# Optimization experiments

Measured on AMD Instinct MI355X. Metric: run time of the kernel, lower is better.

## Reference

```python
import jax, jax.numpy as jnp
import numpy as np

B, T, N, C_IN = 2, 12, 50000, 1
H = 16          # hidden = out channels of STConv
KT = 3          # temporal kernel size
E = 800000      # edges (avg degree 16)
NUM_CLASSES = 2


def _temporal_conv(x, wP, bP, wQ, bQ, wR, bR):
    # Gated temporal conv (GLU): relu(P * sigmoid(Q) + R), 'valid' conv over time.
    # x: (B, Tt, N, C); w*: (KT, C, H)
    Tt = x.shape[1]
    def conv(w, b):
        out = b
        for k in range(KT):  # KT=3, tiny unrolled loop
            out = out + jnp.einsum('btnc,co->btno', x[:, k:Tt - KT + 1 + k], w[k])
        return out
    return jax.nn.relu(conv(wP, bP) * jax.nn.sigmoid(conv(wQ, bQ)) + conv(wR, bR))


def _cheb_conv(x, edge_index, edge_weight, w, b):
    # ChebConv K=2, sym normalization, lambda_max=2:
    #   out  = Tx_0 @ W0 + Tx_1 @ W1 + b
    src, dst = edge_index[0], edge_index[1]
    n = x.shape[2]
    deg = jax.ops.segment_sum(edge_weight, src, num_segments=n)
    dis = jnp.where(deg > 0, jax.lax.rsqrt(jnp.maximum(deg, 1e-12)), 0.0)
    norm = -dis[src] * edge_weight * dis[dst]                    # (E,)
    Bc, Tc, _, Hc = x.shape
    xf = jnp.transpose(x, (2, 0, 1, 3)).reshape(n, -1)           # (N, B*T*H)
    agg = jax.ops.segment_sum(norm[:, None] * xf[src], dst, num_segments=n)
    tx1 = jnp.transpose(agg.reshape(n, Bc, Tc, Hc), (1, 2, 0, 3))  # (B, T, N, H)
    return jnp.einsum('btnc,co->btno', x, w[0]) + jnp.einsum('btnc,co->btno', tx1, w[1]) + b


def _forward(x, edge_index, edge_weight,
             tc1_P_w, tc1_P_b, tc1_Q_w, tc1_Q_b, tc1_R_w, tc1_R_b,
             cheb_w, cheb_b,
             tc2_P_w, tc2_P_b, tc2_Q_w, tc2_Q_b, tc2_R_w, tc2_R_b,
             lin_w, lin_b):
    h = _temporal_conv(x, tc1_P_w, tc1_P_b, tc1_Q_w, tc1_Q_b, tc1_R_w, tc1_R_b)  # (B, T-2, N, H)
    h = jax.nn.relu(_cheb_conv(h, edge_index, edge_weight, cheb_w, cheb_b))
    h = _temporal_conv(h, tc2_P_w, tc2_P_b, tc2_Q_w, tc2_Q_b, tc2_R_w, tc2_R_b)  # (B, T-4, N, H)
    h = h.mean(axis=1)                                                            # (B, N, H)
    return h @ lin_w + lin_b                                                      # (B, N, classes)


def setup_inputs() -> dict:
    key = jax.random.key(0)
    ks = jax.random.split(key, 12)
    x = jax.random.normal(ks[0], (B, T, N, C_IN), jnp.float32)
    edge_index = jax.random.randint(ks[1], (2, E), 0, N, dtype=jnp.int32).astype(jnp.int64)
    edge_weight = jax.random.uniform(ks[2], (E,), jnp.float32)

    def conv_w(k, cin, cout):
        s = 1.0 / np.sqrt(cin * KT)
        return jax.random.uniform(k, (KT, cin, cout), jnp.float32, -s, s)

    inp = {'x': x, 'edge_index': edge_index, 'edge_weight': edge_weight}
    for i, name in enumerate(['tc1_P', 'tc1_Q', 'tc1_R']):
        inp[name + '_w'] = conv_w(ks[3 + i], C_IN, H)
        inp[name + '_b'] = jnp.zeros((H,), jnp.float32)
    for i, name in enumerate(['tc2_P', 'tc2_Q', 'tc2_R']):
        inp[name + '_w'] = conv_w(ks[6 + i], H, H)
        inp[name + '_b'] = jnp.zeros((H,), jnp.float32)
    sc = 1.0 / np.sqrt(H)
    inp['cheb_w'] = jax.random.uniform(ks[9], (2, H, H), jnp.float32, -sc, sc)
    inp['cheb_b'] = jnp.zeros((H,), jnp.float32)
    inp['lin_w'] = jax.random.uniform(ks[10], (H, NUM_CLASSES), jnp.float32, -sc, sc)
    inp['lin_b'] = jnp.zeros((NUM_CLASSES,), jnp.float32)
    return inp


def reference(x, edge_index, edge_weight,
              tc1_P_w, tc1_P_b, tc1_Q_w, tc1_Q_b, tc1_R_w, tc1_R_b,
              tc2_P_w, tc2_P_b, tc2_Q_w, tc2_Q_b, tc2_R_w, tc2_R_b,
              cheb_w, cheb_b, lin_w, lin_b):
    return _forward(x, edge_index, edge_weight,
                    tc1_P_w, tc1_P_b, tc1_Q_w, tc1_Q_b, tc1_R_w, tc1_R_b,
                    cheb_w, cheb_b,
                    tc2_P_w, tc2_P_b, tc2_Q_w, tc2_Q_b, tc2_R_w, tc2_R_b,
                    lin_w, lin_b)
```

## Files before the change

### kernel.cpp

```cpp
#include <hip/hip_runtime.h>

typedef unsigned short ushort_t;
typedef unsigned int uint_t;
typedef __attribute__((ext_vector_type(8))) short short8;
typedef __attribute__((ext_vector_type(4))) float float4v;

constexpr int Bb = 2, Tt = 12, Nn = 50000, Hh = 16, Ee = 800000;
constexpr int T1 = 10, T2 = 8;
constexpr int F = 320;
constexpr int NP = 50176;
constexpr int NXCD = 8;
constexpr int CAP8 = 16;

#define DEV __device__ __forceinline__

DEV float bf2f(ushort_t u) { return __uint_as_float(((uint_t)u) << 16); }
DEV ushort_t f2bf(float f) {
  uint_t u = __float_as_uint(f);
  u += 0x7fffu + ((u >> 16) & 1u);
  return (ushort_t)(u >> 16);
}
DEV float blo(uint_t u) { return __uint_as_float(u << 16); }
DEV float bhi(uint_t u) { return __uint_as_float(u & 0xffff0000u); }
DEV float sigm(float x) { return 1.0f / (1.0f + __expf(-x)); }

DEV int xcc_id() {
  int x;
  asm volatile("s_getreg_b32 %0, hwreg(HW_REG_XCC_ID)" : "=s"(x));
  return x & (NXCD - 1);
}

DEV float loadF(const void* p, int j, int isb) {
  return isb ? bf2f(((const ushort_t*)p)[j]) : ((const float*)p)[j];
}
DEV int loadI(const void* p, long long j, int is64) {
  return is64 ? (int)(((const long long*)p)[j]) : ((const int*)p)[j];
}

__global__ void k_wprep(const void* ew, const void* ei,
                        const void* t1Pw, const void* t1Pb,
                        const void* t1Qw, const void* t1Qb,
                        const void* t1Rw, const void* t1Rb,
                        const void* t2Pw, const void* t2Pb,
                        const void* t2Qw, const void* t2Qb,
                        const void* t2Rw, const void* t2Rb,
                        const void* chw, const void* chb,
                        const void* lw, const void* lb,
                        int* flags, float* W, ushort_t* Bf, uint_t* zero_base) {
  int gid = blockIdx.x * 256 + threadIdx.x;
  if (gid < 16 * NP) zero_base[gid] = 0u;
  if (blockIdx.x != 0) return;

  __shared__ int sflags[2];
  int tid = threadIdx.x;
  if (tid < 64) {
    int lane = tid;
    const ushort_t* u = (const ushort_t*)ew;
    int cnt = 0;
    for (int j = lane; j < 512; j += 64) cnt += (u[j] < 0x3F80u) ? 1 : 0;
#pragma unroll
    for (int d = 32; d; d >>= 1) cnt += __shfl_xor(cnt, d, 64);
    const int* e32 = (const int*)ei;
    int even_nz = 0, odd_nz = 0;
    for (int j = 2 * lane; j < 256; j += 128) {
      even_nz |= (e32[j] != 0);
      odd_nz |= (e32[j + 1] != 0);
    }
    unsigned long long be = __ballot(even_nz), bo = __ballot(odd_nz);
    if (lane == 0) {
      int f0 = (cnt >= 450) ? 1 : 0;
      int f1 = (bo == 0ull && be != 0ull) ? 1 : 0;
      sflags[0] = f0; sflags[1] = f1;
      flags[0] = f0; flags[1] = f1;
    }
  }
  __syncthreads();
  int isb = sflags[0];
#define CVT(src, off, n) for (int j = tid; j < (n); j += 256) W[(off) + j] = loadF(src, j, isb);
  CVT(t1Pw, 0, 48)   CVT(t1Pb, 48, 16)
  CVT(t1Qw, 64, 48)  CVT(t1Qb, 112, 16)
  CVT(t1Rw, 128, 48) CVT(t1Rb, 176, 16)
  CVT(t2Pw, 192, 768)  CVT(t2Pb, 960, 16)
  CVT(t2Qw, 976, 768)  CVT(t2Qb, 1744, 16)
  CVT(t2Rw, 1760, 768) CVT(t2Rb, 2528, 16)
  CVT(chw, 2544, 512)  CVT(chb, 3056, 16)
  CVT(lw, 3072, 32)    CVT(lb, 3104, 2)
#undef CVT
  for (int i = tid; i < 3072; i += 256) {
    int j = i & 7, lane = (i >> 3) & 63, s = (i >> 9) & 1, tau = i >> 10;
    int kap = s * 32 + ((lane >> 4) << 3) + j;
    int nsub = lane & 15;
    ushort_t v = 0;
    if (kap < 48) {
      int kk = kap >> 4, c = kap & 15;
      const void* src = (tau == 0) ? t2Pw : (tau == 1) ? t2Qw : t2Rw;
      v = f2bf(loadF(src, kk * 256 + c * 16 + nsub, isb));
    }
    Bf[i] = v;
  }
}

__global__ __launch_bounds__(256) void k_pre(const void* __restrict__ x,
                                             const void* __restrict__ ei,
                                             const void* __restrict__ ew,
                                             const float* __restrict__ W,
                                             const int* __restrict__ flags,
                                             ushort_t* __restrict__ xfh,
                                             uint_t* __restrict__ deg8,
                                             int* __restrict__ cnt8,
                                             uint_t* __restrict__ ecv8) {
  int id = blockIdx.x * 256 + threadIdx.x;
  int isb = flags[0];
  if (id < Ee) {
    int is64 = flags[1];
    int s = loadI(ei, id, is64), d = loadI(ei, (long long)Ee + id, is64);
    float w = loadF(ew, id, isb);
    int xcd = xcc_id();
    uint_t wq = __float2uint_rn(w * 16777216.0f);
    __hip_atomic_fetch_add(&deg8[xcd * NP + s], wq,
                           __ATOMIC_RELAXED, __HIP_MEMORY_SCOPE_WORKGROUP);
    int pos = __hip_atomic_fetch_add(&cnt8[xcd * NP + d], 1,
                                     __ATOMIC_RELAXED, __HIP_MEMORY_SCOPE_WORKGROUP);
    if (pos < CAP8)
      ecv8[((size_t)xcd * Nn + d) * CAP8 + pos] =
          ((uint_t)s << 16) | (uint_t)f2bf(w);
  }
  if (id < T1 * Nn) {
    int n = id % Nn;
    int t = id / Nn;
    uint_t u[16];
#pragma unroll
    for (int b = 0; b < 2; ++b) {
      float x0 = loadF(x, (b * Tt + t + 0) * Nn + n, isb);
      float x1 = loadF(x, (b * Tt + t + 1) * Nn + n, isb);
      float x2 = loadF(x, (b * Tt + t + 2) * Nn + n, isb);
      ushort_t g[16];
#pragma unroll
      for (int h = 0; h < 16; ++h) {
        float p = W[48 + h] + x0 * W[0 + h] + x1 * W[16 + h] + x2 * W[32 + h];
        float q = W[112 + h] + x0 * W[64 + h] + x1 * W[80 + h] + x2 * W[96 + h];
        float r = W[176 + h] + x0 * W[128 + h] + x1 * W[144 + h] + x2 * W[160 + h];
        g[h] = f2bf(fmaxf(fmaf(p, sigm(q), r), 0.0f));
      }
#pragma unroll
      for (int j = 0; j < 8; ++j)
        u[b * 8 + j] = (uint_t)g[2 * j] | ((uint_t)g[2 * j + 1] << 16);
    }
    uint4* dst = (uint4*)(xfh + (size_t)n * F + t * 32);
    dst[0] = make_uint4(u[0], u[1], u[2], u[3]);
    dst[1] = make_uint4(u[4], u[5], u[6], u[7]);
    dst[2] = make_uint4(u[8], u[9], u[10], u[11]);
    dst[3] = make_uint4(u[12], u[13], u[14], u[15]);
  }
}

__global__ __launch_bounds__(256) void k_dis(uint_t* __restrict__ deg8) {
  int i = blockIdx.x * 256 + threadIdx.x;
  if (i >= Nn) return;
  uint_t v = 0;
#pragma unroll
  for (int j = 0; j < 8; ++j) v += deg8[j * NP + i];
  float f = (float)v * (1.0f / 16777216.0f);
  ((float*)deg8)[i] = (v > 0u) ? (1.0f / sqrtf(fmaxf(f, 1e-12f))) : 0.0f;
}

__global__ __launch_bounds__(256) void k_agg(const int* __restrict__ cnt8,
                                             const uint_t* __restrict__ ecv8,
                                             const float* __restrict__ dis,
                                             const uint2* __restrict__ xf2,
                                             const float* __restrict__ W,
                                             ushort_t* __restrict__ h2) {
  __shared__ float sh[4][640];
  int wid = threadIdx.x >> 6;
  int lane = threadIdx.x & 63;
  int gw = blockIdx.x * 4 + wid;
  int myx = 0, slot = lane, tot = 0;
#pragma unroll
  for (int xx = 0; xx < NXCD; ++xx) {
    int c = min(cnt8[xx * NP + gw], CAP8);
    if (lane >= tot) { myx = xx; slot = lane - tot; }
    tot += c;
  }
  int deg = min(tot, 64);
  int l16 = 64 + (lane & 15);
  float a0 = 0.f, a1 = 0.f, a2 = 0.f, a3 = 0.f;
  float c0 = 0.f, c1 = 0.f, c2 = 0.f, c3 = 0.f;

#define ACC(v, p, q)                                                          \
  a0 = fmaf(v, blo(p.x), a0); a1 = fmaf(v, bhi(p.x), a1);                     \
  a2 = fmaf(v, blo(p.y), a2); a3 = fmaf(v, bhi(p.y), a3);                     \
  c0 = fmaf(v, blo(q.x), c0); c1 = fmaf(v, bhi(q.x), c1);                     \
  c2 = fmaf(v, blo(q.y), c2); c3 = fmaf(v, bhi(q.y), c3);

  int colv = 0;
  int valv_i = 0;
  if (lane < deg) {
    uint_t t = ecv8[((size_t)myx * Nn + gw) * CAP8 + slot];
    int src = t >> 16;
    colv = src * (F * 2);
    valv_i = __float_as_int(bf2f((ushort_t)(t & 0xffffu)) * dis[src]);
  }
  const char* xb = (const char*)xf2;
  int e = 0;
  for (; e + 4 <= deg; e += 4) {
    int b0 = __builtin_amdgcn_readlane(colv, e + 0);
    int b1 = __builtin_amdgcn_readlane(colv, e + 1);
    int b2 = __builtin_amdgcn_readlane(colv, e + 2);
    int b3 = __builtin_amdgcn_readlane(colv, e + 3);
    float v0 = __int_as_float(__builtin_amdgcn_readlane(valv_i, e + 0));
    float v1 = __int_as_float(__builtin_amdgcn_readlane(valv_i, e + 1));
    float v2 = __int_as_float(__builtin_amdgcn_readlane(valv_i, e + 2));
    float v3 = __int_as_float(__builtin_amdgcn_readlane(valv_i, e + 3));
    const uint2* t0 = (const uint2*)(xb + b0);
    const uint2* t1 = (const uint2*)(xb + b1);
    const uint2* t2 = (const uint2*)(xb + b2);
    const uint2* t3 = (const uint2*)(xb + b3);
    uint2 p0 = t0[lane], q0 = t0[l16];
    uint2 p1 = t1[lane], q1 = t1[l16];
    uint2 p2 = t2[lane], q2 = t2[l16];
    uint2 p3 = t3[lane], q3 = t3[l16];
    ACC(v0, p0, q0) ACC(v1, p1, q1) ACC(v2, p2, q2) ACC(v3, p3, q3)
  }
  for (; e < deg; ++e) {
    int b = __builtin_amdgcn_readlane(colv, e);
    float v = __int_as_float(__builtin_amdgcn_readlane(valv_i, e));
    const uint2* tp = (const uint2*)(xb + b);
    uint2 p = tp[lane], q = tp[l16];
    ACC(v, p, q)
  }
#undef ACC

  float nd = -dis[gw];
  float* sa = sh[wid];
  float* sx = sh[wid] + 320;
  const uint2* xrow = xf2 + (size_t)gw * 80;
  uint2 xp = xrow[lane], xq = xrow[l16];
  ((float4*)sa)[lane] = make_float4(a0 * nd, a1 * nd, a2 * nd, a3 * nd);
  ((float4*)sx)[lane] = make_float4(blo(xp.x), bhi(xp.x), blo(xp.y), bhi(xp.y));
  if (lane < 16) {
    ((float4*)sa)[64 + lane] = make_float4(c0 * nd, c1 * nd, c2 * nd, c3 * nd);
    ((float4*)sx)[64 + lane] = make_float4(blo(xq.x), bhi(xq.x), blo(xq.y), bhi(xq.y));
  }
  __builtin_amdgcn_wave_barrier();
  int h = lane & 15;
  float w0[16], w1[16];
#pragma unroll
  for (int c = 0; c < 16; ++c) {
    w0[c] = W[2544 + c * 16 + h];
    w1[c] = W[2800 + c * 16 + h];
  }
  float bias = W[3056 + h];
  ushort_t* orow = h2 + (size_t)gw * F;
#pragma unroll
  for (int j = 0; j < 5; ++j) {
    int base2 = (lane & 48) + 64 * j;
    float o2 = bias;
#pragma unroll
    for (int c = 0; c < 16; ++c)
      o2 = fmaf(sx[base2 + c], w0[c], fmaf(sa[base2 + c], w1[c], o2));
    orow[lane + 64 * j] = f2bf(fmaxf(o2, 0.0f));
  }
}

__global__ __launch_bounds__(256) void k_tc2h(const ushort_t* __restrict__ h2,
                                              const ushort_t* __restrict__ Bf,
                                              const float* __restrict__ W,
                                              float* __restrict__ out) {
  int tid = threadIdx.x;
  int wid = tid >> 6, lane = tid & 63;
  int quad = lane >> 4, hcol = lane & 15;
  short8 bfr[3][2];
#pragma unroll
  for (int tau = 0; tau < 3; ++tau)
#pragma unroll
    for (int s = 0; s < 2; ++s)
      bfr[tau][s] = *(const short8*)(Bf + (tau * 1024 + s * 512 + lane * 8));
  float pb = W[960 + hcol], qb = W[1744 + hcol], rb = W[2528 + hcol];
  float lw0 = W[3072 + 2 * hcol], lw1 = W[3073 + 2 * hcol];
  float ob0 = W[3104], ob1 = W[3105];
  int bm = hcol >> 3, t2m = hcol & 7;
  int kk0 = quad >> 1, off0 = (quad & 1) * 8;
#pragma unroll
  for (int nn = 0; nn < 4; ++nn) {
    int n = blockIdx.x * 16 + wid * 4 + nn;
    const ushort_t* row = h2 + (size_t)n * F;
    short8 a0 = *(const short8*)(row + (t2m + kk0) * 32 + bm * 16 + off0);
    short8 a1 = (short8)0;
    if (quad < 2) a1 = *(const short8*)(row + (t2m + 2) * 32 + bm * 16 + quad * 8);
    float4v accP = {0.f, 0.f, 0.f, 0.f};
    float4v accQ = {0.f, 0.f, 0.f, 0.f};
    float4v accR = {0.f, 0.f, 0.f, 0.f};
    accP = __builtin_amdgcn_mfma_f32_16x16x32_bf16(a0, bfr[0][0], accP, 0, 0, 0);
    accP = __builtin_amdgcn_mfma_f32_16x16x32_bf16(a1, bfr[0][1], accP, 0, 0, 0);
    accQ = __builtin_amdgcn_mfma_f32_16x16x32_bf16(a0, bfr[1][0], accQ, 0, 0, 0);
    accQ = __builtin_amdgcn_mfma_f32_16x16x32_bf16(a1, bfr[1][1], accQ, 0, 0, 0);
    accR = __builtin_amdgcn_mfma_f32_16x16x32_bf16(a0, bfr[2][0], accR, 0, 0, 0);
    accR = __builtin_amdgcn_mfma_f32_16x16x32_bf16(a1, bfr[2][1], accR, 0, 0, 0);
    float s0 = 0.0f;
#pragma unroll
    for (int r = 0; r < 4; ++r) {
      float P = accP[r] + pb, Q = accQ[r] + qb, R = accR[r] + rb;
      s0 += fmaxf(fmaf(P, sigm(Q), R), 0.0f);
    }
    s0 += __shfl_xor(s0, 16);
    float mmean = s0 * 0.125f;
    float u0 = mmean * lw0, u1 = mmean * lw1;
#pragma unroll
    for (int d = 1; d < 16; d <<= 1) {
      u0 += __shfl_xor(u0, d);
      u1 += __shfl_xor(u1, d);
    }
    if ((lane & 31) == 0) {
      int b = lane >> 5;
      ((float2*)out)[(size_t)b * Nn + n] = make_float2(u0 + ob0, u1 + ob1);
    }
  }
}

extern "C" void kernel_launch(void* const* d_in, const int* in_sizes, int n_in,
                              void* d_out, int out_size, void* d_ws, size_t ws_size,
                              hipStream_t stream) {
  (void)in_sizes; (void)n_in; (void)out_size; (void)ws_size;
  const void* x = d_in[0];
  const void* ei = d_in[1];
  const void* ew = d_in[2];

  char* wsb = (char*)d_ws;
  size_t off = 0;
  auto alloc = [&](size_t bytes) -> void* {
    void* p = wsb + off;
    off = (off + bytes + 255) & ~(size_t)255;
    return p;
  };
  int* flags = (int*)alloc(256);
  float* W = (float*)alloc(4096 * 4);
  ushort_t* Bf = (ushort_t*)alloc(3072 * 2);
  uint_t* deg8 = (uint_t*)alloc((size_t)NXCD * NP * 4);
  int* cnt8 = (int*)alloc((size_t)NXCD * NP * 4);
  uint_t* ecv8 = (uint_t*)alloc((size_t)NXCD * Nn * CAP8 * 4);
  ushort_t* xfh = (ushort_t*)alloc((size_t)Nn * F * 2);
  ushort_t* h2 = (ushort_t*)alloc((size_t)Nn * F * 2);

  int zblk = (16 * NP + 255) / 256;
  k_wprep<<<zblk, 256, 0, stream>>>(
      ew, ei,
      d_in[3], d_in[4], d_in[5], d_in[6], d_in[7], d_in[8],
      d_in[9], d_in[10], d_in[11], d_in[12], d_in[13], d_in[14],
      d_in[15], d_in[16], d_in[17], d_in[18], flags, W, Bf, deg8);

  k_pre<<<(Ee + 255) / 256, 256, 0, stream>>>(x, ei, ew, W, flags, xfh, deg8, cnt8, ecv8);
  k_dis<<<(Nn + 255) / 256, 256, 0, stream>>>(deg8);
  k_agg<<<Nn / 4, 256, 0, stream>>>(cnt8, ecv8, (const float*)deg8, (const uint2*)xfh, W, h2);
  k_tc2h<<<Nn / 16, 256, 0, stream>>>(h2, Bf, W, (float*)d_out);
}
```

Measured before the change: 297.4 us.

## Fuse pre, dis, agg, tc2 kernels into one cooperative persistent kernel

Merges the four dependent kernels into a single cooperative kernel that uses grid-stride loops and grid.sync() between phases, replacing separate kernel launches. The grid is sized from occupancy and capped at 1024 blocks. The first temporal-conv phase is also re-indexed so each thread handles one (b,t,n) instead of both batches. This saves launch gaps and tail effects, but it adds grid-wide barrier cost and caps parallelism at a fixed persistent grid, which can lower latency hiding in the gather-heavy aggregation phase.

Measured after the change: 720.5 us. 2.42x slower.

```diff
diff --git a/kernel.cpp b/kernel.cpp
--- a/kernel.cpp
+++ b/kernel.cpp
@@ -1,4 +1,7 @@
 #include <hip/hip_runtime.h>
+#include <hip/hip_cooperative_groups.h>
+
+namespace cg = cooperative_groups;
 
 typedef unsigned short ushort_t;
 typedef unsigned int uint_t;
@@ -100,91 +103,88 @@
   }
 }
 
-__global__ __launch_bounds__(256) void k_pre(const void* __restrict__ x,
-                                             const void* __restrict__ ei,
-                                             const void* __restrict__ ew,
-                                             const float* __restrict__ W,
-                                             const int* __restrict__ flags,
-                                             ushort_t* __restrict__ xfh,
-                                             uint_t* __restrict__ deg8,
-                                             int* __restrict__ cnt8,
-                                             uint_t* __restrict__ ecv8) {
-  int id = blockIdx.x * 256 + threadIdx.x;
-  int isb = flags[0];
-  if (id < Ee) {
-    int is64 = flags[1];
-    int s = loadI(ei, id, is64), d = loadI(ei, (long long)Ee + id, is64);
-    float w = loadF(ew, id, isb);
-    int xcd = xcc_id();
-    uint_t wq = __float2uint_rn(w * 16777216.0f);
-    __hip_atomic_fetch_add(&deg8[xcd * NP + s], wq,
-                           __ATOMIC_RELAXED, __HIP_MEMORY_SCOPE_WORKGROUP);
-    int pos = __hip_atomic_fetch_add(&cnt8[xcd * NP + d], 1,
-                                     __ATOMIC_RELAXED, __HIP_MEMORY_SCOPE_WORKGROUP);
-    if (pos < CAP8)
-      ecv8[((size_t)xcd * Nn + d) * CAP8 + pos] =
-          ((uint_t)s << 16) | (uint_t)f2bf(w);
-  }
-  if (id < T1 * Nn) {
-    int n = id % Nn;
-    int t = id / Nn;
-    uint_t u[16];
-#pragma unroll
-    for (int b = 0; b < 2; ++b) {
-      float x0 = loadF(x, (b * Tt + t + 0) * Nn + n, isb);
-      float x1 = loadF(x, (b * Tt + t + 1) * Nn + n, isb);
-      float x2 = loadF(x, (b * Tt + t + 2) * Nn + n, isb);
-      ushort_t g[16];
-#pragma unroll
-      for (int h = 0; h < 16; ++h) {
-        float p = W[48 + h] + x0 * W[0 + h] + x1 * W[16 + h] + x2 * W[32 + h];
-        float q = W[112 + h] + x0 * W[64 + h] + x1 * W[80 + h] + x2 * W[96 + h];
-        float r = W[176 + h] + x0 * W[128 + h] + x1 * W[144 + h] + x2 * W[160 + h];
-        g[h] = f2bf(fmaxf(fmaf(p, sigm(q), r), 0.0f));
-      }
-#pragma unroll
-      for (int j = 0; j < 8; ++j)
-        u[b * 8 + j] = (uint_t)g[2 * j] | ((uint_t)g[2 * j + 1] << 16);
-    }
-    uint4* dst = (uint4*)(xfh + (size_t)n * F + t * 32);
-    dst[0] = make_uint4(u[0], u[1], u[2], u[3]);
-    dst[1] = make_uint4(u[4], u[5], u[6], u[7]);
-    dst[2] = make_uint4(u[8], u[9], u[10], u[11]);
-    dst[3] = make_uint4(u[12], u[13], u[14], u[15]);
-  }
-}
-
-__global__ __launch_bounds__(256) void k_dis(uint_t* __restrict__ deg8) {
-  int i = blockIdx.x * 256 + threadIdx.x;
-  if (i >= Nn) return;
-  uint_t v = 0;
-#pragma unroll
-  for (int j = 0; j < 8; ++j) v += deg8[j * NP + i];
-  float f = (float)v * (1.0f / 16777216.0f);
-  ((float*)deg8)[i] = (v > 0u) ? (1.0f / sqrtf(fmaxf(f, 1e-12f))) : 0.0f;
-}
-
-__global__ __launch_bounds__(256) void k_agg(const int* __restrict__ cnt8,
-                                             const uint_t* __restrict__ ecv8,
-                                             const float* __restrict__ dis,
-                                             const uint2* __restrict__ xf2,
-                                             const float* __restrict__ W,
-                                             ushort_t* __restrict__ h2) {
+__global__ __launch_bounds__(256, 4) void k_mega(
+    const void* __restrict__ x, const void* __restrict__ ei,
+    const void* __restrict__ ew, const float* __restrict__ W,
+    const int* __restrict__ flags, ushort_t* xfh, uint_t* deg8,
+    int* cnt8, uint_t* ecv8, ushort_t* h2,
+    const ushort_t* __restrict__ Bf, float* out) {
+  cg::grid_group grid = cg::this_grid();
   __shared__ float sh[4][640];
-  int wid = threadIdx.x >> 6;
-  int lane = threadIdx.x & 63;
-  int gw = blockIdx.x * 4 + wid;
-  int myx = 0, slot = lane, tot = 0;
-#pragma unroll
-  for (int xx = 0; xx < NXCD; ++xx) {
-    int c = min(cnt8[xx * NP + gw], CAP8);
-    if (lane >= tot) { myx = xx; slot = lane - tot; }
-    tot += c;
-  }
-  int deg = min(tot, 64);
-  int l16 = 64 + (lane & 15);
-  float a0 = 0.f, a1 = 0.f, a2 = 0.f, a3 = 0.f;
-  float c0 = 0.f, c1 = 0.f, c2 = 0.f, c3 = 0.f;
+  const int tid = threadIdx.x;
+  const int gid0 = blockIdx.x * 256 + tid;
+  const int GS = gridDim.x * 256;
+  const int isb = flags[0], is64 = flags[1];
+  const int wid = tid >> 6, lane = tid & 63;
+
+  {
+    const int xcd = xcc_id();
+    for (int id = gid0; id < Bb * T1 * Nn; id += GS) {
+      if (id < Ee) {
+        int s = loadI(ei, id, is64), d = loadI(ei, (long long)Ee + id, is64);
+        float w = loadF(ew, id, isb);
+        uint_t wq = __float2uint_rn(w * 16777216.0f);
+        __hip_atomic_fetch_add(&deg8[xcd * NP + s], wq,
+                               __ATOMIC_RELAXED, __HIP_MEMORY_SCOPE_WORKGROUP);
+        int pos = __hip_atomic_fetch_add(&cnt8[xcd * NP + d], 1,
+                                         __ATOMIC_RELAXED, __HIP_MEMORY_SCOPE_WORKGROUP);
+        if (pos < CAP8)
+          ecv8[((size_t)xcd * Nn + d) * CAP8 + pos] =
+              ((uint_t)s << 16) | (uint_t)f2bf(w);
+      }
+      {
+        int n = id % Nn;
+        int bt = id / Nn;
+        int t = bt % T1, b = bt / T1;
+        float x0 = loadF(x, (b * Tt + t + 0) * Nn + n, isb);
+        float x1 = loadF(x, (b * Tt + t + 1) * Nn + n, isb);
+        float x2 = loadF(x, (b * Tt + t + 2) * Nn + n, isb);
+        ushort_t g[16];
+#pragma unroll
+        for (int h = 0; h < 16; ++h) {
+          float p = W[48 + h] + x0 * W[0 + h] + x1 * W[16 + h] + x2 * W[32 + h];
+          float q = W[112 + h] + x0 * W[64 + h] + x1 * W[80 + h] + x2 * W[96 + h];
+          float r = W[176 + h] + x0 * W[128 + h] + x1 * W[144 + h] + x2 * W[160 + h];
+          g[h] = f2bf(fmaxf(fmaf(p, sigm(q), r), 0.0f));
+        }
+        uint_t u[8];
+#pragma unroll
+        for (int j = 0; j < 8; ++j)
+          u[j] = (uint_t)g[2 * j] | ((uint_t)g[2 * j + 1] << 16);
+        uint4* dst = (uint4*)(xfh + (size_t)n * F + t * 32 + b * 16);
+        dst[0] = make_uint4(u[0], u[1], u[2], u[3]);
+        dst[1] = make_uint4(u[4], u[5], u[6], u[7]);
+      }
+    }
+  }
+  __threadfence();
+  grid.sync();
+
+  for (int i = gid0; i < Nn; i += GS) {
+    uint_t v = 0;
+#pragma unroll
+    for (int j = 0; j < 8; ++j) v += deg8[j * NP + i];
+    float f = (float)v * (1.0f / 16777216.0f);
+    ((float*)deg8)[i] = (v > 0u) ? (1.0f / sqrtf(fmaxf(f, 1e-12f))) : 0.0f;
+  }
+  __threadfence();
+  grid.sync();
+
+  {
+    const float* dis = (const float*)deg8;
+    const uint2* xf2 = (const uint2*)xfh;
+    const int l16 = 64 + (lane & 15);
+    for (int gw = blockIdx.x * 4 + wid; gw < Nn; gw += gridDim.x * 4) {
+      int myx = 0, slot = lane, tot = 0;
+#pragma unroll
+      for (int xx = 0; xx < NXCD; ++xx) {
+        int c = min(cnt8[xx * NP + gw], CAP8);
+        if (lane >= tot) { myx = xx; slot = lane - tot; }
+        tot += c;
+      }
+      int deg = min(tot, 64);
+      float a0 = 0.f, a1 = 0.f, a2 = 0.f, a3 = 0.f;
+      float c0 = 0.f, c1 = 0.f, c2 = 0.f, c3 = 0.f;
 
 #define ACC(v, p, q)                                                          \
   a0 = fmaf(v, blo(p.x), a0); a1 = fmaf(v, bhi(p.x), a1);                     \
@@ -192,127 +192,128 @@
   c0 = fmaf(v, blo(q.x), c0); c1 = fmaf(v, bhi(q.x), c1);                     \
   c2 = fmaf(v, blo(q.y), c2); c3 = fmaf(v, bhi(q.y), c3);
 
-  int colv = 0;
-  int valv_i = 0;
-  if (lane < deg) {
-    uint_t t = ecv8[((size_t)myx * Nn + gw) * CAP8 + slot];
-    int src = t >> 16;
-    colv = src * (F * 2);
-    valv_i = __float_as_int(bf2f((ushort_t)(t & 0xffffu)) * dis[src]);
-  }
-  const char* xb = (const char*)xf2;
-  int e = 0;
-  for (; e + 4 <= deg; e += 4) {
-    int b0 = __builtin_amdgcn_readlane(colv, e + 0);
-    int b1 = __builtin_amdgcn_readlane(colv, e + 1);
-    int b2 = __builtin_amdgcn_readlane(colv, e + 2);
-    int b3 = __builtin_amdgcn_readlane(colv, e + 3);
-    float v0 = __int_as_float(__builtin_amdgcn_readlane(valv_i, e + 0));
-    float v1 = __int_as_float(__builtin_amdgcn_readlane(valv_i, e + 1));
-    float v2 = __int_as_float(__builtin_amdgcn_readlane(valv_i, e + 2));
-    float v3 = __int_as_float(__builtin_amdgcn_readlane(valv_i, e + 3));
-    const uint2* t0 = (const uint2*)(xb + b0);
-    const uint2* t1 = (const uint2*)(xb + b1);
-    const uint2* t2 = (const uint2*)(xb + b2);
-    const uint2* t3 = (const uint2*)(xb + b3);
-    uint2 p0 = t0[lane], q0 = t0[l16];
-    uint2 p1 = t1[lane], q1 = t1[l16];
-    uint2 p2 = t2[lane], q2 = t2[l16];
-    uint2 p3 = t3[lane], q3 = t3[l16];
-    ACC(v0, p0, q0) ACC(v1, p1, q1) ACC(v2, p2, q2) ACC(v3, p3, q3)
-  }
-  for (; e < deg; ++e) {
-    int b = __builtin_amdgcn_readlane(colv, e);
-    float v = __int_as_float(__builtin_amdgcn_readlane(valv_i, e));
-    const uint2* tp = (const uint2*)(xb + b);
-    uint2 p = tp[lane], q = tp[l16];
-    ACC(v, p, q)
-  }
+      int colv = 0;
+      int valv_i = 0;
+      if (lane < deg) {
+        uint_t t = ecv8[((size_t)myx * Nn + gw) * CAP8 + slot];
+        int src = t >> 16;
+        colv = src * (F * 2);
+        valv_i = __float_as_int(bf2f((ushort_t)(t & 0xffffu)) * dis[src]);
+      }
+      const char* xb = (const char*)xf2;
+      int e = 0;
+      for (; e + 4 <= deg; e += 4) {
+        int b0 = __builtin_amdgcn_readlane(colv, e + 0);
+        int b1 = __builtin_amdgcn_readlane(colv, e + 1);
+        int b2 = __builtin_amdgcn_readlane(colv, e + 2);
+        int b3 = __builtin_amdgcn_readlane(colv, e + 3);
+        float v0 = __int_as_float(__builtin_amdgcn_readlane(valv_i, e + 0));
+        float v1 = __int_as_float(__builtin_amdgcn_readlane(valv_i, e + 1));
+        float v2 = __int_as_float(__builtin_amdgcn_readlane(valv_i, e + 2));
+        float v3 = __int_as_float(__builtin_amdgcn_readlane(valv_i, e + 3));
+        const uint2* t0 = (const uint2*)(xb + b0);
+        const uint2* t1 = (const uint2*)(xb + b1);
+        const uint2* t2 = (const uint2*)(xb + b2);
+        const uint2* t3 = (const uint2*)(xb + b3);
+        uint2 p0 = t0[lane], q0 = t0[l16];
+        uint2 p1 = t1[lane], q1 = t1[l16];
+        uint2 p2 = t2[lane], q2 = t2[l16];
+        uint2 p3 = t3[lane], q3 = t3[l16];
+        ACC(v0, p0, q0) ACC(v1, p1, q1) ACC(v2, p2, q2) ACC(v3, p3, q3)
+      }
+      for (; e < deg; ++e) {
+        int b = __builtin_amdgcn_readlane(colv, e);
+        float v = __int_as_float(__builtin_amdgcn_readlane(valv_i, e));
+        const uint2* tp = (const uint2*)(xb + b);
+        uint2 p = tp[lane], q = tp[l16];
+        ACC(v, p, q)
+      }
 #undef ACC
 
-  float nd = -dis[gw];
-  float* sa = sh[wid];
-  float* sx = sh[wid] + 320;
-  const uint2* xrow = xf2 + (size_t)gw * 80;
-  uint2 xp = xrow[lane], xq = xrow[l16];
-  ((float4*)sa)[lane] = make_float4(a0 * nd, a1 * nd, a2 * nd, a3 * nd);
-  ((float4*)sx)[lane] = make_float4(blo(xp.x), bhi(xp.x), blo(xp.y), bhi(xp.y));
-  if (lane < 16) {
-    ((float4*)sa)[64 + lane] = make_float4(c0 * nd, c1 * nd, c2 * nd, c3 * nd);
-    ((float4*)sx)[64 + lane] = make_float4(blo(xq.x), bhi(xq.x), blo(xq.y), bhi(xq.y));
-  }
-  __builtin_amdgcn_wave_barrier();
-  int h = lane & 15;
-  float w0[16], w1[16];
-#pragma unroll
-  for (int c = 0; c < 16; ++c) {
-    w0[c] = W[2544 + c * 16 + h];
-    w1[c] = W[2800 + c * 16 + h];
-  }
-  float bias = W[3056 + h];
-  ushort_t* orow = h2 + (size_t)gw * F;
-#pragma unroll
-  for (int j = 0; j < 5; ++j) {
-    int base2 = (lane & 48) + 64 * j;
-    float o2 = bias;
-#pragma unroll
-    for (int c = 0; c < 16; ++c)
-      o2 = fmaf(sx[base2 + c], w0[c], fmaf(sa[base2 + c], w1[c], o2));
-    orow[lane + 64 * j] = f2bf(fmaxf(o2, 0.0f));
-  }
-}
-
-__global__ __launch_bounds__(256) void k_tc2h(const ushort_t* __restrict__ h2,
-                                              const ushort_t* __restrict__ Bf,
-                                              const float* __restrict__ W,
-                                              float* __restrict__ out) {
-  int tid = threadIdx.x;
-  int wid = tid >> 6, lane = tid & 63;
-  int quad = lane >> 4, hcol = lane & 15;
-  short8 bfr[3][2];
-#pragma unroll
-  for (int tau = 0; tau < 3; ++tau)
-#pragma unroll
-    for (int s = 0; s < 2; ++s)
-      bfr[tau][s] = *(const short8*)(Bf + (tau * 1024 + s * 512 + lane * 8));
-  float pb = W[960 + hcol], qb = W[1744 + hcol], rb = W[2528 + hcol];
-  float lw0 = W[3072 + 2 * hcol], lw1 = W[3073 + 2 * hcol];
-  float ob0 = W[3104], ob1 = W[3105];
-  int bm = hcol >> 3, t2m = hcol & 7;
-  int kk0 = quad >> 1, off0 = (quad & 1) * 8;
-#pragma unroll
-  for (int nn = 0; nn < 4; ++nn) {
-    int n = blockIdx.x * 16 + wid * 4 + nn;
-    const ushort_t* row = h2 + (size_t)n * F;
-    short8 a0 = *(const short8*)(row + (t2m + kk0) * 32 + bm * 16 + off0);
-    short8 a1 = (short8)0;
-    if (quad < 2) a1 = *(const short8*)(row + (t2m + 2) * 32 + bm * 16 + quad * 8);
-    float4v accP = {0.f, 0.f, 0.f, 0.f};
-    float4v accQ = {0.f, 0.f, 0.f, 0.f};
-    float4v accR = {0.f, 0.f, 0.f, 0.f};
-    accP = __builtin_amdgcn_mfma_f32_16x16x32_bf16(a0, bfr[0][0], accP, 0, 0, 0);
-    accP = __builtin_amdgcn_mfma_f32_16x16x32_bf16(a1, bfr[0][1], accP, 0, 0, 0);
-    accQ = __builtin_amdgcn_mfma_f32_16x16x32_bf16(a0, bfr[1][0], accQ, 0, 0, 0);
-    accQ = __builtin_amdgcn_mfma_f32_16x16x32_bf16(a1, bfr[1][1], accQ, 0, 0, 0);
-    accR = __builtin_amdgcn_mfma_f32_16x16x32_bf16(a0, bfr[2][0], accR, 0, 0, 0);
-    accR = __builtin_amdgcn_mfma_f32_16x16x32_bf16(a1, bfr[2][1], accR, 0, 0, 0);
-    float s0 = 0.0f;
-#pragma unroll
-    for (int r = 0; r < 4; ++r) {
-      float P = accP[r] + pb, Q = accQ[r] + qb, R = accR[r] + rb;
-      s0 += fmaxf(fmaf(P, sigm(Q), R), 0.0f);
-    }
-    s0 += __shfl_xor(s0, 16);
-    float mmean = s0 * 0.125f;
-    float u0 = mmean * lw0, u1 = mmean * lw1;
-#pragma unroll
-    for (int d = 1; d < 16; d <<= 1) {
-      u0 += __shfl_xor(u0, d);
-      u1 += __shfl_xor(u1, d);
-    }
-    if ((lane & 31) == 0) {
-      int b = lane >> 5;
-      ((float2*)out)[(size_t)b * Nn + n] = make_float2(u0 + ob0, u1 + ob1);
+      float nd = -dis[gw];
+      float* sa = sh[wid];
+      float* sx = sh[wid] + 320;
+      const uint2* xrow = xf2 + (size_t)gw * 80;
+      uint2 xp = xrow[lane], xq = xrow[l16];
+      ((float4*)sa)[lane] = make_float4(a0 * nd, a1 * nd, a2 * nd, a3 * nd);
+      ((float4*)sx)[lane] = make_float4(blo(xp.x), bhi(xp.x), blo(xp.y), bhi(xp.y));
+      if (lane < 16) {
+        ((float4*)sa)[64 + lane] = make_float4(c0 * nd, c1 * nd, c2 * nd, c3 * nd);
+        ((float4*)sx)[64 + lane] = make_float4(blo(xq.x), bhi(xq.x), blo(xq.y), bhi(xq.y));
+      }
+      __builtin_amdgcn_wave_barrier();
+      int h = lane & 15;
+      float w0[16], w1[16];
+#pragma unroll
+      for (int c = 0; c < 16; ++c) {
+        w0[c] = W[2544 + c * 16 + h];
+        w1[c] = W[2800 + c * 16 + h];
+      }
+      float bias = W[3056 + h];
+      ushort_t* orow = h2 + (size_t)gw * F;
+#pragma unroll
+      for (int j = 0; j < 5; ++j) {
+        int base2 = (lane & 48) + 64 * j;
+        float o2 = bias;
+#pragma unroll
+        for (int c = 0; c < 16; ++c)
+          o2 = fmaf(sx[base2 + c], w0[c], fmaf(sa[base2 + c], w1[c], o2));
+        orow[lane + 64 * j] = f2bf(fmaxf(o2, 0.0f));
+      }
+    }
+  }
+  __threadfence();
+  grid.sync();
+
+  {
+    const int quad = lane >> 4, hcol = lane & 15;
+    short8 bfr[3][2];
+#pragma unroll
+    for (int tau = 0; tau < 3; ++tau)
+#pragma unroll
+      for (int s = 0; s < 2; ++s)
+        bfr[tau][s] = *(const short8*)(Bf + (tau * 1024 + s * 512 + lane * 8));
+    float pb = W[960 + hcol], qb = W[1744 + hcol], rb = W[2528 + hcol];
+    float lw0 = W[3072 + 2 * hcol], lw1 = W[3073 + 2 * hcol];
+    float ob0 = W[3104], ob1 = W[3105];
+    int bm = hcol >> 3, t2m = hcol & 7;
+    int kk0 = quad >> 1, off0 = (quad & 1) * 8;
+    for (int grp = blockIdx.x; grp < Nn / 16; grp += gridDim.x) {
+#pragma unroll
+      for (int nn = 0; nn < 4; ++nn) {
+        int n = grp * 16 + wid * 4 + nn;
+        const ushort_t* row = h2 + (size_t)n * F;
+        short8 a0 = *(const short8*)(row + (t2m + kk0) * 32 + bm * 16 + off0);
+        short8 a1 = (short8)0;
+        if (quad < 2) a1 = *(const short8*)(row + (t2m + 2) * 32 + bm * 16 + quad * 8);
+        float4v accP = {0.f, 0.f, 0.f, 0.f};
+        float4v accQ = {0.f, 0.f, 0.f, 0.f};
+        float4v accR = {0.f, 0.f, 0.f, 0.f};
+        accP = __builtin_amdgcn_mfma_f32_16x16x32_bf16(a0, bfr[0][0], accP, 0, 0, 0);
+        accP = __builtin_amdgcn_mfma_f32_16x16x32_bf16(a1, bfr[0][1], accP, 0, 0, 0);
+        accQ = __builtin_amdgcn_mfma_f32_16x16x32_bf16(a0, bfr[1][0], accQ, 0, 0, 0);
+        accQ = __builtin_amdgcn_mfma_f32_16x16x32_bf16(a1, bfr[1][1], accQ, 0, 0, 0);
+        accR = __builtin_amdgcn_mfma_f32_16x16x32_bf16(a0, bfr[2][0], accR, 0, 0, 0);
+        accR = __builtin_amdgcn_mfma_f32_16x16x32_bf16(a1, bfr[2][1], accR, 0, 0, 0);
+        float s0 = 0.0f;
+#pragma unroll
+        for (int r = 0; r < 4; ++r) {
+          float P = accP[r] + pb, Q = accQ[r] + qb, R = accR[r] + rb;
+          s0 += fmaxf(fmaf(P, sigm(Q), R), 0.0f);
+        }
+        s0 += __shfl_xor(s0, 16);
+        float mmean = s0 * 0.125f;
+        float u0 = mmean * lw0, u1 = mmean * lw1;
+#pragma unroll
+        for (int d = 1; d < 16; d <<= 1) {
+          u0 += __shfl_xor(u0, d);
+          u1 += __shfl_xor(u1, d);
+        }
+        if ((lane & 31) == 0) {
+          int b = lane >> 5;
+          ((float2*)out)[(size_t)b * Nn + n] = make_float2(u0 + ob0, u1 + ob1);
+        }
+      }
     }
   }
 }
@@ -340,6 +341,7 @@
   uint_t* ecv8 = (uint_t*)alloc((size_t)NXCD * Nn * CAP8 * 4);
   ushort_t* xfh = (ushort_t*)alloc((size_t)Nn * F * 2);
   ushort_t* h2 = (ushort_t*)alloc((size_t)Nn * F * 2);
+  float* outf = (float*)d_out;
 
   int zblk = (16 * NP + 255) / 256;
   k_wprep<<<zblk, 256, 0, stream>>>(
@@ -348,8 +350,13 @@
       d_in[9], d_in[10], d_in[11], d_in[12], d_in[13], d_in[14],
       d_in[15], d_in[16], d_in[17], d_in[18], flags, W, Bf, deg8);
 
-  k_pre<<<(Ee + 255) / 256, 256, 0, stream>>>(x, ei, ew, W, flags, xfh, deg8, cnt8, ecv8);
-  k_dis<<<(Nn + 255) / 256, 256, 0, stream>>>(deg8);
-  k_agg<<<Nn / 4, 256, 0, stream>>>(cnt8, ecv8, (const float*)deg8, (const uint2*)xfh, W, h2);
-  k_tc2h<<<Nn / 16, 256, 0, stream>>>(h2, Bf, W, (float*)d_out);
-}
+  int maxb = 0;
+  if (hipOccupancyMaxActiveBlocksPerMultiprocessor(&maxb, k_mega, 256, 0) != hipSuccess || maxb < 1)
+    maxb = 2;
+  int grid = 256 * maxb;
+  if (grid > 1024) grid = 1024;
+  void* ka[] = {(void*)&x,    (void*)&ei,   (void*)&ew,   (void*)&W,
+                (void*)&flags, (void*)&xfh, (void*)&deg8, (void*)&cnt8,
+                (void*)&ecv8, (void*)&h2,   (void*)&Bf,   (void*)&outf};
+  hipLaunchCooperativeKernel((void*)k_mega, dim3(grid), dim3(256), ka, 0, stream);
+}
```

## Fuse second temporal conv and head into aggregation kernel via LDS

Applied to the files above, without the earlier changes.

The ChebConv output per node is kept in shared memory and fed straight into the MFMA-based second gated temporal conv, mean and linear head inside the aggregation kernel. This removes the h2 intermediate buffer and its global write and read round trip, plus one kernel launch. Separately, the first temporal conv in the preprocessing kernel is split so each thread handles one (batch, time, node) instead of both batches, and the grid grows to cover it. Costs are a heavier aggregation kernel with more registers and LDS per block, and per-wave reloads of the B fragments and weights.

After: 278.4 us (median of 2 runs). -6.4%, faster.

```diff
diff --git a/kernel.cpp b/kernel.cpp
--- a/kernel.cpp
+++ b/kernel.cpp
@@ -125,32 +125,27 @@
       ecv8[((size_t)xcd * Nn + d) * CAP8 + pos] =
           ((uint_t)s << 16) | (uint_t)f2bf(w);
   }
-  if (id < T1 * Nn) {
+  if (id < Bb * T1 * Nn) {
     int n = id % Nn;
-    int t = id / Nn;
-    uint_t u[16];
-#pragma unroll
-    for (int b = 0; b < 2; ++b) {
-      float x0 = loadF(x, (b * Tt + t + 0) * Nn + n, isb);
-      float x1 = loadF(x, (b * Tt + t + 1) * Nn + n, isb);
-      float x2 = loadF(x, (b * Tt + t + 2) * Nn + n, isb);
-      ushort_t g[16];
-#pragma unroll
-      for (int h = 0; h < 16; ++h) {
-        float p = W[48 + h] + x0 * W[0 + h] + x1 * W[16 + h] + x2 * W[32 + h];
-        float q = W[112 + h] + x0 * W[64 + h] + x1 * W[80 + h] + x2 * W[96 + h];
-        float r = W[176 + h] + x0 * W[128 + h] + x1 * W[144 + h] + x2 * W[160 + h];
-        g[h] = f2bf(fmaxf(fmaf(p, sigm(q), r), 0.0f));
-      }
-#pragma unroll
-      for (int j = 0; j < 8; ++j)
-        u[b * 8 + j] = (uint_t)g[2 * j] | ((uint_t)g[2 * j + 1] << 16);
-    }
-    uint4* dst = (uint4*)(xfh + (size_t)n * F + t * 32);
+    int bt = id / Nn;
+    int t = bt % T1, b = bt / T1;
+    float x0 = loadF(x, (b * Tt + t + 0) * Nn + n, isb);
+    float x1 = loadF(x, (b * Tt + t + 1) * Nn + n, isb);
+    float x2 = loadF(x, (b * Tt + t + 2) * Nn + n, isb);
+    ushort_t g[16];
+#pragma unroll
+    for (int h = 0; h < 16; ++h) {
+      float p = W[48 + h] + x0 * W[0 + h] + x1 * W[16 + h] + x2 * W[32 + h];
+      float q = W[112 + h] + x0 * W[64 + h] + x1 * W[80 + h] + x2 * W[96 + h];
+      float r = W[176 + h] + x0 * W[128 + h] + x1 * W[144 + h] + x2 * W[160 + h];
+      g[h] = f2bf(fmaxf(fmaf(p, sigm(q), r), 0.0f));
+    }
+    uint_t u[8];
+#pragma unroll
+    for (int j = 0; j < 8; ++j) u[j] = (uint_t)g[2 * j] | ((uint_t)g[2 * j + 1] << 16);
+    uint4* dst = (uint4*)(xfh + (size_t)n * F + t * 32 + b * 16);
     dst[0] = make_uint4(u[0], u[1], u[2], u[3]);
     dst[1] = make_uint4(u[4], u[5], u[6], u[7]);
-    dst[2] = make_uint4(u[8], u[9], u[10], u[11]);
-    dst[3] = make_uint4(u[12], u[13], u[14], u[15]);
   }
 }
 
@@ -169,8 +164,10 @@
                                              const float* __restrict__ dis,
                                              const uint2* __restrict__ xf2,
                                              const float* __restrict__ W,
-                                             ushort_t* __restrict__ h2) {
+                                             const ushort_t* __restrict__ Bf,
+                                             float* __restrict__ out) {
   __shared__ float sh[4][640];
+  __shared__ ushort_t sh2[4][320];
   int wid = threadIdx.x >> 6;
   int lane = threadIdx.x & 63;
   int gw = blockIdx.x * 4 + wid;
@@ -243,59 +240,53 @@
   }
   __builtin_amdgcn_wave_barrier();
   int h = lane & 15;
-  float w0[16], w1[16];
-#pragma unroll
-  for (int c = 0; c < 16; ++c) {
-    w0[c] = W[2544 + c * 16 + h];
-    w1[c] = W[2800 + c * 16 + h];
-  }
-  float bias = W[3056 + h];
-  ushort_t* orow = h2 + (size_t)gw * F;
-#pragma unroll
-  for (int j = 0; j < 5; ++j) {
-    int base2 = (lane & 48) + 64 * j;
-    float o2 = bias;
-#pragma unroll
-    for (int c = 0; c < 16; ++c)
-      o2 = fmaf(sx[base2 + c], w0[c], fmaf(sa[base2 + c], w1[c], o2));
-    orow[lane + 64 * j] = f2bf(fmaxf(o2, 0.0f));
-  }
-}
-
-__global__ __launch_bounds__(256) void k_tc2h(const ushort_t* __restrict__ h2,
-                                              const ushort_t* __restrict__ Bf,
-                                              const float* __restrict__ W,
-                                              float* __restrict__ out) {
-  int tid = threadIdx.x;
-  int wid = tid >> 6, lane = tid & 63;
-  int quad = lane >> 4, hcol = lane & 15;
-  short8 bfr[3][2];
-#pragma unroll
-  for (int tau = 0; tau < 3; ++tau)
-#pragma unroll
-    for (int s = 0; s < 2; ++s)
-      bfr[tau][s] = *(const short8*)(Bf + (tau * 1024 + s * 512 + lane * 8));
-  float pb = W[960 + hcol], qb = W[1744 + hcol], rb = W[2528 + hcol];
-  float lw0 = W[3072 + 2 * hcol], lw1 = W[3073 + 2 * hcol];
-  float ob0 = W[3104], ob1 = W[3105];
-  int bm = hcol >> 3, t2m = hcol & 7;
-  int kk0 = quad >> 1, off0 = (quad & 1) * 8;
-#pragma unroll
-  for (int nn = 0; nn < 4; ++nn) {
-    int n = blockIdx.x * 16 + wid * 4 + nn;
-    const ushort_t* row = h2 + (size_t)n * F;
-    short8 a0 = *(const short8*)(row + (t2m + kk0) * 32 + bm * 16 + off0);
-    short8 a1 = (short8)0;
-    if (quad < 2) a1 = *(const short8*)(row + (t2m + 2) * 32 + bm * 16 + quad * 8);
+  {
+    float w0[16], w1[16];
+#pragma unroll
+    for (int c = 0; c < 16; ++c) {
+      w0[c] = W[2544 + c * 16 + h];
+      w1[c] = W[2800 + c * 16 + h];
+    }
+    float bias = W[3056 + h];
+    ushort_t* s2 = sh2[wid];
+#pragma unroll
+    for (int j = 0; j < 5; ++j) {
+      int base2 = (lane & 48) + 64 * j;
+      float o2 = bias;
+#pragma unroll
+      for (int c = 0; c < 16; ++c)
+        o2 = fmaf(sx[base2 + c], w0[c], fmaf(sa[base2 + c], w1[c], o2));
+      s2[lane + 64 * j] = f2bf(fmaxf(o2, 0.0f));
+    }
+  }
+  __builtin_amdgcn_wave_barrier();
+
+  {
+    const ushort_t* s2 = sh2[wid];
+    int quad = lane >> 4, hcol = h;
+    int bm = hcol >> 3, t2m = hcol & 7;
+    int kk0 = quad >> 1, off0 = (quad & 1) * 8;
+    short8 a0f = *(const short8*)(s2 + (t2m + kk0) * 32 + bm * 16 + off0);
+    short8 a1f = (short8)0;
+    if (quad < 2) a1f = *(const short8*)(s2 + (t2m + 2) * 32 + bm * 16 + quad * 8);
+    short8 bfr[3][2];
+#pragma unroll
+    for (int tau = 0; tau < 3; ++tau)
+#pragma unroll
+      for (int s = 0; s < 2; ++s)
+        bfr[tau][s] = *(const short8*)(Bf + (tau * 1024 + s * 512 + lane * 8));
+    float pb = W[960 + hcol], qb = W[1744 + hcol], rb = W[2528 + hcol];
+    float lw0 = W[3072 + 2 * hcol], lw1 = W[3073 + 2 * hcol];
+    float ob0 = W[3104], ob1 = W[3105];
     float4v accP = {0.f, 0.f, 0.f, 0.f};
     float4v accQ = {0.f, 0.f, 0.f, 0.f};
     float4v accR = {0.f, 0.f, 0.f, 0.f};
-    accP = __builtin_amdgcn_mfma_f32_16x16x32_bf16(a0, bfr[0][0], accP, 0, 0, 0);
-    accP = __builtin_amdgcn_mfma_f32_16x16x32_bf16(a1, bfr[0][1], accP, 0, 0, 0);
-    accQ = __builtin_amdgcn_mfma_f32_16x16x32_bf16(a0, bfr[1][0], accQ, 0, 0, 0);
-    accQ = __builtin_amdgcn_mfma_f32_16x16x32_bf16(a1, bfr[1][1], accQ, 0, 0, 0);
-    accR = __builtin_amdgcn_mfma_f32_16x16x32_bf16(a0, bfr[2][0], accR, 0, 0, 0);
-    accR = __builtin_amdgcn_mfma_f32_16x16x32_bf16(a1, bfr[2][1], accR, 0, 0, 0);
+    accP = __builtin_amdgcn_mfma_f32_16x16x32_bf16(a0f, bfr[0][0], accP, 0, 0, 0);
+    accP = __builtin_amdgcn_mfma_f32_16x16x32_bf16(a1f, bfr[0][1], accP, 0, 0, 0);
+    accQ = __builtin_amdgcn_mfma_f32_16x16x32_bf16(a0f, bfr[1][0], accQ, 0, 0, 0);
+    accQ = __builtin_amdgcn_mfma_f32_16x16x32_bf16(a1f, bfr[1][1], accQ, 0, 0, 0);
+    accR = __builtin_amdgcn_mfma_f32_16x16x32_bf16(a0f, bfr[2][0], accR, 0, 0, 0);
+    accR = __builtin_amdgcn_mfma_f32_16x16x32_bf16(a1f, bfr[2][1], accR, 0, 0, 0);
     float s0 = 0.0f;
 #pragma unroll
     for (int r = 0; r < 4; ++r) {
@@ -312,7 +303,7 @@
     }
     if ((lane & 31) == 0) {
       int b = lane >> 5;
-      ((float2*)out)[(size_t)b * Nn + n] = make_float2(u0 + ob0, u1 + ob1);
+      ((float2*)out)[(size_t)b * Nn + gw] = make_float2(u0 + ob0, u1 + ob1);
     }
   }
 }
@@ -339,7 +330,6 @@
   int* cnt8 = (int*)alloc((size_t)NXCD * NP * 4);
   uint_t* ecv8 = (uint_t*)alloc((size_t)NXCD * Nn * CAP8 * 4);
   ushort_t* xfh = (ushort_t*)alloc((size_t)Nn * F * 2);
-  ushort_t* h2 = (ushort_t*)alloc((size_t)Nn * F * 2);
 
   int zblk = (16 * NP + 255) / 256;
   k_wprep<<<zblk, 256, 0, stream>>>(
@@ -348,8 +338,8 @@
       d_in[9], d_in[10], d_in[11], d_in[12], d_in[13], d_in[14],
       d_in[15], d_in[16], d_in[17], d_in[18], flags, W, Bf, deg8);
 
-  k_pre<<<(Ee + 255) / 256, 256, 0, stream>>>(x, ei, ew, W, flags, xfh, deg8, cnt8, ecv8);
+  k_pre<<<(Bb * T1 * Nn + 255) / 256, 256, 0, stream>>>(x, ei, ew, W, flags, xfh, deg8, cnt8, ecv8);
   k_dis<<<(Nn + 255) / 256, 256, 0, stream>>>(deg8);
-  k_agg<<<Nn / 4, 256, 0, stream>>>(cnt8, ecv8, (const float*)deg8, (const uint2*)xfh, W, h2);
-  k_tc2h<<<Nn / 16, 256, 0, stream>>>(h2, Bf, W, (float*)d_out);
-}
+  k_agg<<<Nn / 4, 256, 0, stream>>>(cnt8, ecv8, (const float*)deg8, (const uint2*)xfh, W, Bf,
+                                    (float*)d_out);
+}
```
